# Optimization experiments

Measured on AMD Instinct MI355X. Metric: run time of the kernel, lower is better.

The kernel has to match this reference:

```python
import jax, jax.numpy as jnp
import numpy as np

EMB = 768
N_HEADS = 12
HEAD_DIM = EMB // N_HEADS


def setup_inputs() -> dict:
    key = jax.random.key(0)
    k_x, k_w1, k_b1, k_w2, k_b2 = jax.random.split(key, 5)
    B, T = 8, 1024
    s = 0.02
    return {
        "x": jax.random.normal(k_x, (B, T, EMB), dtype=jnp.float32),
        "w_attn": jax.random.normal(k_w1, (EMB, 3 * EMB), dtype=jnp.float32) * s,
        "b_attn": jax.random.normal(k_b1, (3 * EMB,), dtype=jnp.float32) * s,
        "w_proj": jax.random.normal(k_w2, (EMB, EMB), dtype=jnp.float32) * s,
        "b_proj": jax.random.normal(k_b2, (EMB,), dtype=jnp.float32) * s,
    }


def reference(x, w_attn, b_attn, w_proj, b_proj):
    B, T, C = x.shape
    qkv = x @ w_attn + b_attn                       # [B,T,3C]
    q, k, v = jnp.split(qkv, 3, axis=2)
    # [B,T,C] -> [B,H,T,D]
    q = q.reshape(B, T, N_HEADS, HEAD_DIM).transpose(0, 2, 1, 3)
    k = k.reshape(B, T, N_HEADS, HEAD_DIM).transpose(0, 2, 1, 3)
    v = v.reshape(B, T, N_HEADS, HEAD_DIM).transpose(0, 2, 1, 3)
    scale = HEAD_DIM ** -0.5
    att = jnp.einsum("bhqd,bhkd->bhqk", q, k) * scale  # [B,H,T,T]
    causal = jnp.tril(jnp.ones((T, T), dtype=bool))
    att = jnp.where(causal, att, -jnp.inf)
    att = jax.nn.softmax(att, axis=-1)
    out = jnp.einsum("bhqk,bhkd->bhqd", att, v)        # [B,H,T,D]
    out = out.transpose(0, 2, 1, 3).reshape(B, T, C)
    return out @ w_proj + b_proj
```

## Files before the change

kernel.cpp:

```cpp
#include <hip/hip_runtime.h>
#include <hip/hip_bf16.h>
#include <math.h>

#define BATCH 8
#define SEQ   1024
#define EMB   768
#define NH    12
#define HD    64
#define QKVW  (3 * EMB)
#define VOFF  (2 * EMB)

typedef short short8   __attribute__((ext_vector_type(8)));
typedef float floatx4  __attribute__((ext_vector_type(4)));

__device__ __forceinline__ short f2bf(float f) {
    union { float f; unsigned u; } v; v.f = f;
    unsigned r = (v.u + 0x7fffu + ((v.u >> 16) & 1u)) >> 16;
    return (short)r;
}

__device__ __forceinline__ void async_load16(const void* g, void* l) {
    __builtin_amdgcn_global_load_lds(
        (const __attribute__((address_space(1))) unsigned int*)g,
        (__attribute__((address_space(3))) unsigned int*)l, 16, 0, 0);
}

__global__ __launch_bounds__(256) void cvt_bf16(
    const float* __restrict__ in, short* __restrict__ out, int n8)
{
    const int i = blockIdx.x * 256 + threadIdx.x;
    if (i >= n8) return;
    const float4 a = ((const float4*)in)[2 * i];
    const float4 b = ((const float4*)in)[2 * i + 1];
    short8 s;
    s[0] = f2bf(a.x); s[1] = f2bf(a.y); s[2] = f2bf(a.z); s[3] = f2bf(a.w);
    s[4] = f2bf(b.x); s[5] = f2bf(b.y); s[6] = f2bf(b.z); s[7] = f2bf(b.w);
    ((short8*)out)[i] = s;
}

__global__ __launch_bounds__(256) void transpose_to_bf16(
    const float* __restrict__ in, short* __restrict__ outT, int R, int C)
{
    __shared__ float t[32][33];
    const int c0 = blockIdx.x * 32, r0 = blockIdx.y * 32;
    const int lx = threadIdx.x & 31, ly = threadIdx.x >> 5;
    #pragma unroll
    for (int i = 0; i < 32; i += 8)
        t[ly + i][lx] = in[(size_t)(r0 + ly + i) * C + c0 + lx];
    __syncthreads();
    #pragma unroll
    for (int i = 0; i < 32; i += 8)
        outT[(size_t)(c0 + ly + i) * R + r0 + lx] = f2bf(t[lx][ly + i]);
}

#define GBK 64

template <int MODE>
__global__ __launch_bounds__(256) void gemm_bf16(
    const short* __restrict__ A, const short* __restrict__ Bt,
    const float* __restrict__ bias, void* __restrict__ Cout,
    short* __restrict__ vt, int M, int N, int K)
{
    __shared__ __align__(16) short As[128 * GBK];
    __shared__ __align__(16) short Bs[128 * GBK];

    const int tid  = threadIdx.x;
    const int wave = tid >> 6;
    const int lane = tid & 63;
    const int ln15 = lane & 15;
    const int quad = lane >> 4;
    const int wr   = (wave >> 1) * 64;
    const int wc   = (wave & 1) * 64;
    const int row0 = blockIdx.y * 128;
    const int col0 = blockIdx.x * 128;

    const bool trans = (MODE == 0) || (col0 < VOFF);

    floatx4 acc[4][4];
    #pragma unroll
    for (int i = 0; i < 4; ++i)
        #pragma unroll
        for (int j = 0; j < 4; ++j) acc[i][j] = (floatx4){0.f, 0.f, 0.f, 0.f};

    for (int k0 = 0; k0 < K; k0 += GBK) {
        __syncthreads();
        #pragma unroll
        for (int p = 0; p < 4; ++p) {
            const int id  = p * 256 + tid;
            const int row = id >> 3;
            const int c   = (id & 7) ^ (row & 7);
            async_load16(A  + (size_t)(row0 + row) * K + k0 + c * 8, &As[id * 8]);
            async_load16(Bt + (size_t)(col0 + row) * K + k0 + c * 8, &Bs[id * 8]);
        }
        __syncthreads();

        #pragma unroll
        for (int half = 0; half < 2; ++half) {
            short8 af[4], bf[4];
            #pragma unroll
            for (int t = 0; t < 4; ++t) {
                const int ch = ((quad + half * 4) ^ (ln15 & 7)) * 8;
                af[t] = *(const short8*)&As[(wr + t * 16 + ln15) * GBK + ch];
                bf[t] = *(const short8*)&Bs[(wc + t * 16 + ln15) * GBK + ch];
            }
            if (trans) {
                #pragma unroll
                for (int i = 0; i < 4; ++i)
                    #pragma unroll
                    for (int j = 0; j < 4; ++j)
                        acc[i][j] = __builtin_amdgcn_mfma_f32_16x16x32_bf16(bf[j], af[i], acc[i][j], 0, 0, 0);
            } else {
                #pragma unroll
                for (int i = 0; i < 4; ++i)
                    #pragma unroll
                    for (int j = 0; j < 4; ++j)
                        acc[i][j] = __builtin_amdgcn_mfma_f32_16x16x32_bf16(af[i], bf[j], acc[i][j], 0, 0, 0);
            }
        }
    }

    if (MODE == 1 && !trans) {
        #pragma unroll
        for (int j = 0; j < 4; ++j) {
            const int c  = col0 + wc + j * 16 + ln15;
            const float bv = bias[c];
            const int c2 = c - VOFF;
            #pragma unroll
            for (int i = 0; i < 4; ++i) {
                const int r = row0 + wr + i * 16 + quad * 4;
                union { short s[4]; unsigned long long u; } pk;
                #pragma unroll
                for (int reg = 0; reg < 4; ++reg)
                    pk.s[reg] = f2bf(acc[i][j][reg] + bv);
                *(unsigned long long*)&vt[(size_t)(r >> 10) * (EMB * SEQ) +
                                          (size_t)c2 * SEQ + (r & 1023)] = pk.u;
            }
        }
    } else {
        float4 b4[4];
        #pragma unroll
        for (int j = 0; j < 4; ++j)
            b4[j] = *(const float4*)&bias[col0 + wc + j * 16 + quad * 4];
        #pragma unroll
        for (int i = 0; i < 4; ++i) {
            const int r = row0 + wr + i * 16 + ln15;
            #pragma unroll
            for (int j = 0; j < 4; ++j) {
                const int c = col0 + wc + j * 16 + quad * 4;
                if (MODE == 1) {
                    union { short s[4]; unsigned long long u; } pk;
                    pk.s[0] = f2bf(acc[i][j][0] + b4[j].x);
                    pk.s[1] = f2bf(acc[i][j][1] + b4[j].y);
                    pk.s[2] = f2bf(acc[i][j][2] + b4[j].z);
                    pk.s[3] = f2bf(acc[i][j][3] + b4[j].w);
                    *(unsigned long long*)&((short*)Cout)[(size_t)r * N + c] = pk.u;
                } else {
                    float4 v;
                    v.x = acc[i][j][0] + b4[j].x;
                    v.y = acc[i][j][1] + b4[j].y;
                    v.z = acc[i][j][2] + b4[j].z;
                    v.w = acc[i][j][3] + b4[j].w;
                    *(float4*)&((float*)Cout)[(size_t)r * N + c] = v;
                }
            }
        }
    }
}

#define NT12 (EMB / 64)

#define BAR()    do { asm volatile("" ::: "memory"); __builtin_amdgcn_s_barrier(); \
                      asm volatile("" ::: "memory"); } while (0)
#define LGKM0()  asm volatile("s_waitcnt lgkmcnt(0)" ::: "memory")
#define VMC0()   asm volatile("s_waitcnt vmcnt(0)" ::: "memory")
#define VMC8()   asm volatile("s_waitcnt vmcnt(8)" ::: "memory")
#define SCHED0() __builtin_amdgcn_sched_barrier(0)
#define PRIO1()  __builtin_amdgcn_s_setprio(1)
#define PRIO0()  __builtin_amdgcn_s_setprio(0)

#define LDA(bf_, r_, q_) (*(const short8*)&As[bf_][(r_) * 64 + ((((q_)) ^ ((r_) & 7)) << 3)])
#define LDB(bf_, r_, q_) (*(const short8*)&Bs[bf_][(r_) * 64 + ((((q_)) ^ ((r_) & 7)) << 3)])

#define MMA_T(IB, JB)                                                        \
    _Pragma("unroll")                                                        \
    for (int kk = 0; kk < 2; ++kk)                                           \
        _Pragma("unroll")                                                    \
        for (int mi = 0; mi < 4; ++mi)                                       \
            _Pragma("unroll")                                                \
            for (int nj = 0; nj < 2; ++nj)                                   \
                acc[(IB) + mi][(JB) + nj] =                                  \
                    __builtin_amdgcn_mfma_f32_16x16x32_bf16(                 \
                        b[(JB) + nj][kk], a[mi][kk],                         \
                        acc[(IB) + mi][(JB) + nj], 0, 0, 0);

#define MMA_D(IB, JB)                                                        \
    _Pragma("unroll")                                                        \
    for (int kk = 0; kk < 2; ++kk)                                           \
        _Pragma("unroll")                                                    \
        for (int mi = 0; mi < 4; ++mi)                                       \
            _Pragma("unroll")                                                \
            for (int nj = 0; nj < 2; ++nj)                                   \
                acc[(IB) + mi][(JB) + nj] =                                  \
                    __builtin_amdgcn_mfma_f32_16x16x32_bf16(                 \
                        a[mi][kk], b[(JB) + nj][kk],                         \
                        acc[(IB) + mi][(JB) + nj], 0, 0, 0);

#define KLOOP(MM)                                                            \
    for (int kt = 0; kt < NT12; ++kt) {                                      \
        const int buf = kt & 1;                                              \
                    \
        _Pragma("unroll")                                                    \
        for (int mi = 0; mi < 4; ++mi)                                       \
            _Pragma("unroll")                                                \
            for (int kk = 0; kk < 2; ++kk)                                   \
                a[mi][kk] = LDA(buf, ar0 + mi * 16, quad + kk * 4);          \
        _Pragma("unroll")                                                    \
        for (int nj = 0; nj < 2; ++nj)                                       \
            _Pragma("unroll")                                                \
            for (int kk = 0; kk < 2; ++kk)                                   \
                b[nj][kk] = LDB(buf, br0 + nj * 16, quad + kk * 4);          \
        BAR(); LGKM0(); SCHED0();                                            \
        PRIO1(); MM(0, 0); PRIO0();                                          \
        BAR();                                                               \
                                    \
        _Pragma("unroll")                                                    \
        for (int nj = 2; nj < 4; ++nj)                                       \
            _Pragma("unroll")                                                \
            for (int kk = 0; kk < 2; ++kk)                                   \
                b[nj][kk] = LDB(buf, br0 + nj * 16, quad + kk * 4);          \
        BAR(); LGKM0(); SCHED0();                                            \
        PRIO1(); MM(0, 2); PRIO0();                                          \
        BAR();                                                               \
             \
        _Pragma("unroll")                                                    \
        for (int mi = 0; mi < 4; ++mi)                                       \
            _Pragma("unroll")                                                \
            for (int kk = 0; kk < 2; ++kk)                                   \
                a[mi][kk] = LDA(buf, ar0 + 64 + mi * 16, quad + kk * 4);     \
        stage_half(kt + 2, 2); stage_half(kt + 2, 3);                        \
        BAR(); LGKM0(); SCHED0();                                            \
        PRIO1(); MM(4, 2); PRIO0();                                          \
        BAR();                                                               \
                           \
        stage_half(kt + 2, 0); stage_half(kt + 2, 1);                        \
        SCHED0();                                                            \
        PRIO1(); MM(4, 0); PRIO0();                                          \
        if (kt + 2 < NT12) { VMC8(); } else { VMC0(); }                      \
        BAR();                                                               \
    }

__global__ __launch_bounds__(512, 2) void gemm_qkv_256(
    const short* __restrict__ A, const short* __restrict__ Bt,
    const float* __restrict__ bias, short* __restrict__ qkvb,
    short* __restrict__ vt)
{
    __shared__ __align__(16) short As[2][256 * 64];
    __shared__ __align__(16) short Bs[2][256 * 64];

    const int tid  = threadIdx.x;
    const int wave = tid >> 6;
    const int lane = tid & 63;
    const int ln15 = lane & 15;
    const int quad = lane >> 4;
    const int wm   = wave >> 2;
    const int wn   = wave & 3;

    const int orig = blockIdx.x;
    const int wg   = (orig & 7) * 36 + (orig >> 3);
    const int bx   = wg % (QKVW / 256);
    const int by   = wg / (QKVW / 256);
    const int row0 = by * 256;
    const int col0 = bx * 256;
    const bool vpath = (col0 >= VOFF);

    const short* Ag = A  + (size_t)row0 * EMB;
    const short* Bg = Bt + (size_t)col0 * EMB;

    auto stage_half = [&](int t, int h) {
        if (t >= NT12) return;
        const int buf   = t & 1;
        const int k0    = t * 64;
        const int rbase = (h & 1) * 128;
        short* lb       = (h < 2) ? &As[buf][rbase * 64] : &Bs[buf][rbase * 64];
        const short* gb = (h < 2) ? Ag : Bg;
        #pragma unroll
        for (int p = 0; p < 2; ++p) {
            const int id  = p * 512 + tid;
            const int row = rbase + (id >> 3);
            const int c   = (id & 7) ^ (row & 7);
            async_load16(gb + (size_t)row * EMB + k0 + c * 8, lb + (size_t)id * 8);
        }
    };

    floatx4 acc[8][4];
    #pragma unroll
    for (int i = 0; i < 8; ++i)
        #pragma unroll
        for (int j = 0; j < 4; ++j) acc[i][j] = (floatx4){0.f, 0.f, 0.f, 0.f};

    short8 a[4][2];
    short8 b[4][2];

    #pragma unroll
    for (int h = 0; h < 4; ++h) stage_half(0, h);
    #pragma unroll
    for (int h = 0; h < 4; ++h) stage_half(1, h);
    VMC8();
    BAR();

    const int ar0 = wm * 128 + ln15;
    const int br0 = wn * 64 + ln15;

    if (vpath) { KLOOP(MMA_D) } else { KLOOP(MMA_T) }

    if (!vpath) {
        #pragma unroll
        for (int j = 0; j < 4; ++j) {
            const float4 b4 = *(const float4*)&bias[col0 + wn * 64 + j * 16 + quad * 4];
            #pragma unroll
            for (int i = 0; i < 8; ++i) {
                const int r = row0 + wm * 128 + i * 16 + ln15;
                const int c = col0 + wn * 64 + j * 16 + quad * 4;
                union { short s[4]; unsigned long long u; } pk;
                pk.s[0] = f2bf(acc[i][j][0] + b4.x);
                pk.s[1] = f2bf(acc[i][j][1] + b4.y);
                pk.s[2] = f2bf(acc[i][j][2] + b4.z);
                pk.s[3] = f2bf(acc[i][j][3] + b4.w);
                *(unsigned long long*)&qkvb[(size_t)r * QKVW + c] = pk.u;
            }
        }
    } else {
        #pragma unroll
        for (int j = 0; j < 4; ++j) {
            const int c  = col0 + wn * 64 + j * 16 + ln15;
            const float bv = bias[c];
            const int c2 = c - VOFF;
            #pragma unroll
            for (int i = 0; i < 8; ++i) {
                const int r = row0 + wm * 128 + i * 16 + quad * 4;
                union { short s[4]; unsigned long long u; } pk;
                #pragma unroll
                for (int reg = 0; reg < 4; ++reg)
                    pk.s[reg] = f2bf(acc[i][j][reg] + bv);
                *(unsigned long long*)&vt[(size_t)(r >> 10) * (EMB * SEQ) +
                                          (size_t)c2 * SEQ + (r & 1023)] = pk.u;
            }
        }
    }
}

#define LDK 72

__global__ __launch_bounds__(256) void attn_mfma(
    const short* __restrict__ qkv, const short* __restrict__ vt,
    short* __restrict__ out)
{
    __shared__ __align__(16) short Ks[64 * LDK];
    __shared__ __align__(16) short Vt[64 * LDK];
    __shared__ __align__(16) short Ps[4 * 16 * LDK];

    const int tid  = threadIdx.x;
    const int wave = tid >> 6;
    const int lane = tid & 63;
    const int ln15 = lane & 15;
    const int quad = lane >> 4;

    const int qc = 15 - (int)(blockIdx.x / (BATCH * NH));
    const int bh = blockIdx.x % (BATCH * NH);
    const int h  = bh % NH;
    const int b  = bh / NH;

    const int q0w = qc * 64 + wave * 16;

    const short* qkv_b = qkv + (size_t)b * SEQ * QKVW + h * HD;
    const short* Kg  = qkv_b + EMB;
    const short* Vtg = vt + ((size_t)b * EMB + h * HD) * SEQ;

    short8 qf[2];
    {
        const short* qrow = qkv_b + (size_t)(q0w + ln15) * QKVW;
        qf[0] = *(const short8*)(qrow + quad * 8);
        qf[1] = *(const short8*)(qrow + quad * 8 + 32);
    }

    floatx4 o[4];
    #pragma unroll
    for (int i = 0; i < 4; ++i) o[i] = (floatx4){0.f, 0.f, 0.f, 0.f};
    float lp[4] = {0.f, 0.f, 0.f, 0.f};

    const int rr = tid >> 3;
    const int c8 = (tid & 7) * 8;

    for (int kt = 0; kt <= qc; ++kt) {
        #pragma unroll
        for (int p = 0; p < 2; ++p) {
            const int r2 = rr + p * 32;
            *(uint4*)&Ks[r2 * LDK + c8] =
                *(const uint4*)(Kg + (size_t)(kt * 64 + r2) * QKVW + c8);
            *(uint4*)&Vt[r2 * LDK + c8] =
                *(const uint4*)(Vtg + (size_t)r2 * SEQ + kt * 64 + c8);
        }
        __syncthreads();

        floatx4 s[4];
        #pragma unroll
        for (int i = 0; i < 4; ++i) s[i] = (floatx4){0.f, 0.f, 0.f, 0.f};
        #pragma unroll
        for (int st = 0; st < 2; ++st)
            #pragma unroll
            for (int sub = 0; sub < 4; ++sub) {
                const short8 kf = *(const short8*)&Ks[(ln15 + sub * 16) * LDK + quad * 8 + st * 32];
                s[sub] = __builtin_amdgcn_mfma_f32_16x16x32_bf16(qf[st], kf, s[sub], 0, 0, 0);
            }

        const bool diag = (kt == qc);
        #pragma unroll
        for (int sub = 0; sub < 4; ++sub)
            #pragma unroll
            for (int reg = 0; reg < 4; ++reg) {
                float pv = __expf(s[sub][reg] * 0.125f);
                if (diag && (ln15 + sub * 16 > wave * 16 + quad * 4 + reg)) pv = 0.f;
                s[sub][reg] = pv;
            }
        #pragma unroll
        for (int reg = 0; reg < 4; ++reg)
            lp[reg] += (s[0][reg] + s[1][reg]) + (s[2][reg] + s[3][reg]);

        short* Pw = &Ps[wave * 16 * LDK];
        #pragma unroll
        for (int sub = 0; sub < 4; ++sub)
            #pragma unroll
            for (int reg = 0; reg < 4; ++reg) {
                const int qr   = quad * 4 + reg;
                const int kr8  = sub * 2 + (ln15 >> 3);
                const int slot = (kr8 + 5 * quad + reg) & 7;
                Pw[qr * LDK + slot * 8 + (ln15 & 7)] = f2bf(s[sub][reg]);
            }

        short8 pf[2];
        #pragma unroll
        for (int st = 0; st < 2; ++st) {
            const int slot = ((quad + 4 * st) + 5 * (ln15 >> 2) + (ln15 & 3)) & 7;
            pf[st] = *(const short8*)&Pw[ln15 * LDK + slot * 8];
        }

        #pragma unroll
        for (int st = 0; st < 2; ++st)
            #pragma unroll
            for (int sub = 0; sub < 4; ++sub) {
                const short8 vf = *(const short8*)&Vt[(ln15 + sub * 16) * LDK + quad * 8 + st * 32];
                o[sub] = __builtin_amdgcn_mfma_f32_16x16x32_bf16(pf[st], vf, o[sub], 0, 0, 0);
            }

        __syncthreads();
    }

    #pragma unroll
    for (int reg = 0; reg < 4; ++reg) {
        float t = lp[reg];
        #pragma unroll
        for (int off = 1; off <= 8; off <<= 1)
            t += __shfl_xor(t, off, 64);
        const float inv = 1.0f / t;
        const size_t row = (size_t)(b * SEQ + q0w + quad * 4 + reg) * EMB + h * HD;
        #pragma unroll
        for (int sub = 0; sub < 4; ++sub)
            out[row + ln15 + sub * 16] = f2bf(o[sub][reg] * inv);
    }
}

extern "C" void kernel_launch(void* const* d_in, const int* in_sizes, int n_in,
                              void* d_out, int out_size, void* d_ws, size_t ws_size,
                              hipStream_t stream)
{
    const float* x      = (const float*)d_in[0];
    const float* w_attn = (const float*)d_in[1];
    const float* b_attn = (const float*)d_in[2];
    const float* w_proj = (const float*)d_in[3];
    const float* b_proj = (const float*)d_in[4];
    float* out = (float*)d_out;

    const int M = BATCH * SEQ;

    short* xb    = (short*)d_ws;
    short* waT   = xb    + (size_t)M * EMB;
    short* wpT   = waT   + (size_t)QKVW * EMB;
    short* qkvb  = wpT   + (size_t)EMB * EMB;
    short* vtb   = qkvb  + (size_t)M * QKVW;
    short* attnb = vtb   + (size_t)BATCH * EMB * SEQ;

    dim3 blk(256);

    cvt_bf16<<<dim3((M * EMB) / 8 / 256), blk, 0, stream>>>(x, xb, (M * EMB) / 8);
    transpose_to_bf16<<<dim3(QKVW / 32, EMB / 32), blk, 0, stream>>>(w_attn, waT, EMB, QKVW);
    transpose_to_bf16<<<dim3(EMB / 32, EMB / 32), blk, 0, stream>>>(w_proj, wpT, EMB, EMB);

    gemm_qkv_256<<<dim3((QKVW / 256) * (M / 256)), dim3(512), 0, stream>>>(
        xb, waT, b_attn, qkvb, vtb);

    attn_mfma<<<dim3(16 * BATCH * NH), blk, 0, stream>>>(qkvb, vtb, attnb);

    gemm_bf16<0><<<dim3(EMB / 128, M / 128), blk, 0, stream>>>(
        attnb, wpT, b_proj, out, nullptr, M, EMB, EMB);
}
```

Before: 216.1 us.

## Replace projection GEMM with double-buffered 128x192 tile kernel using six waves

The output projection GEMM moves from a simple single-buffered 128x128 kernel with 4 waves to a new kernel with 128x192 tiles, 6 waves, and double-buffered LDS. Loads for the next K tile are staged asynchronously and overlap the MFMA work through split A/B staging, explicit waitcnt and barriers, and priority hints. Workgroup IDs are also remapped for L2 locality. The goal is to hide global-load latency and improve data reuse. The cost is more LDS per block and fragile hand-written synchronisation.

```diff
diff --git a/kernel.cpp b/kernel.cpp
--- a/kernel.cpp
+++ b/kernel.cpp
@@ -53,130 +53,18 @@
         outT[(size_t)(c0 + ly + i) * R + r0 + lx] = f2bf(t[lx][ly + i]);
 }
 
-#define GBK 64
-
-template <int MODE>
-__global__ __launch_bounds__(256) void gemm_bf16(
-    const short* __restrict__ A, const short* __restrict__ Bt,
-    const float* __restrict__ bias, void* __restrict__ Cout,
-    short* __restrict__ vt, int M, int N, int K)
-{
-    __shared__ __align__(16) short As[128 * GBK];
-    __shared__ __align__(16) short Bs[128 * GBK];
-
-    const int tid  = threadIdx.x;
-    const int wave = tid >> 6;
-    const int lane = tid & 63;
-    const int ln15 = lane & 15;
-    const int quad = lane >> 4;
-    const int wr   = (wave >> 1) * 64;
-    const int wc   = (wave & 1) * 64;
-    const int row0 = blockIdx.y * 128;
-    const int col0 = blockIdx.x * 128;
-
-    const bool trans = (MODE == 0) || (col0 < VOFF);
-
-    floatx4 acc[4][4];
-    #pragma unroll
-    for (int i = 0; i < 4; ++i)
-        #pragma unroll
-        for (int j = 0; j < 4; ++j) acc[i][j] = (floatx4){0.f, 0.f, 0.f, 0.f};
-
-    for (int k0 = 0; k0 < K; k0 += GBK) {
-        __syncthreads();
-        #pragma unroll
-        for (int p = 0; p < 4; ++p) {
-            const int id  = p * 256 + tid;
-            const int row = id >> 3;
-            const int c   = (id & 7) ^ (row & 7);
-            async_load16(A  + (size_t)(row0 + row) * K + k0 + c * 8, &As[id * 8]);
-            async_load16(Bt + (size_t)(col0 + row) * K + k0 + c * 8, &Bs[id * 8]);
-        }
-        __syncthreads();
-
-        #pragma unroll
-        for (int half = 0; half < 2; ++half) {
-            short8 af[4], bf[4];
-            #pragma unroll
-            for (int t = 0; t < 4; ++t) {
-                const int ch = ((quad + half * 4) ^ (ln15 & 7)) * 8;
-                af[t] = *(const short8*)&As[(wr + t * 16 + ln15) * GBK + ch];
-                bf[t] = *(const short8*)&Bs[(wc + t * 16 + ln15) * GBK + ch];
-            }
-            if (trans) {
-                #pragma unroll
-                for (int i = 0; i < 4; ++i)
-                    #pragma unroll
-                    for (int j = 0; j < 4; ++j)
-                        acc[i][j] = __builtin_amdgcn_mfma_f32_16x16x32_bf16(bf[j], af[i], acc[i][j], 0, 0, 0);
-            } else {
-                #pragma unroll
-                for (int i = 0; i < 4; ++i)
-                    #pragma unroll
-                    for (int j = 0; j < 4; ++j)
-                        acc[i][j] = __builtin_amdgcn_mfma_f32_16x16x32_bf16(af[i], bf[j], acc[i][j], 0, 0, 0);
-            }
-        }
-    }
-
-    if (MODE == 1 && !trans) {
-        #pragma unroll
-        for (int j = 0; j < 4; ++j) {
-            const int c  = col0 + wc + j * 16 + ln15;
-            const float bv = bias[c];
-            const int c2 = c - VOFF;
-            #pragma unroll
-            for (int i = 0; i < 4; ++i) {
-                const int r = row0 + wr + i * 16 + quad * 4;
-                union { short s[4]; unsigned long long u; } pk;
-                #pragma unroll
-                for (int reg = 0; reg < 4; ++reg)
-                    pk.s[reg] = f2bf(acc[i][j][reg] + bv);
-                *(unsigned long long*)&vt[(size_t)(r >> 10) * (EMB * SEQ) +
-                                          (size_t)c2 * SEQ + (r & 1023)] = pk.u;
-            }
-        }
-    } else {
-        float4 b4[4];
-        #pragma unroll
-        for (int j = 0; j < 4; ++j)
-            b4[j] = *(const float4*)&bias[col0 + wc + j * 16 + quad * 4];
-        #pragma unroll
-        for (int i = 0; i < 4; ++i) {
-            const int r = row0 + wr + i * 16 + ln15;
-            #pragma unroll
-            for (int j = 0; j < 4; ++j) {
-                const int c = col0 + wc + j * 16 + quad * 4;
-                if (MODE == 1) {
-                    union { short s[4]; unsigned long long u; } pk;
-                    pk.s[0] = f2bf(acc[i][j][0] + b4[j].x);
-                    pk.s[1] = f2bf(acc[i][j][1] + b4[j].y);
-                    pk.s[2] = f2bf(acc[i][j][2] + b4[j].z);
-                    pk.s[3] = f2bf(acc[i][j][3] + b4[j].w);
-                    *(unsigned long long*)&((short*)Cout)[(size_t)r * N + c] = pk.u;
-                } else {
-                    float4 v;
-                    v.x = acc[i][j][0] + b4[j].x;
-                    v.y = acc[i][j][1] + b4[j].y;
-                    v.z = acc[i][j][2] + b4[j].z;
-                    v.w = acc[i][j][3] + b4[j].w;
-                    *(float4*)&((float*)Cout)[(size_t)r * N + c] = v;
-                }
-            }
-        }
-    }
-}
-
 #define NT12 (EMB / 64)
 
 #define BAR()    do { asm volatile("" ::: "memory"); __builtin_amdgcn_s_barrier(); \
                       asm volatile("" ::: "memory"); } while (0)
 #define LGKM0()  asm volatile("s_waitcnt lgkmcnt(0)" ::: "memory")
 #define VMC0()   asm volatile("s_waitcnt vmcnt(0)" ::: "memory")
+#define VMC4()   asm volatile("s_waitcnt vmcnt(4)" ::: "memory")
 #define VMC8()   asm volatile("s_waitcnt vmcnt(8)" ::: "memory")
 #define SCHED0() __builtin_amdgcn_sched_barrier(0)
 #define PRIO1()  __builtin_amdgcn_s_setprio(1)
 #define PRIO0()  __builtin_amdgcn_s_setprio(0)
+
 
 #define LDA(bf_, r_, q_) (*(const short8*)&As[bf_][(r_) * 64 + ((((q_)) ^ ((r_) & 7)) << 3)])
 #define LDB(bf_, r_, q_) (*(const short8*)&Bs[bf_][(r_) * 64 + ((((q_)) ^ ((r_) & 7)) << 3)])
@@ -349,6 +237,143 @@
     }
 }
 
+
+#define LDA8(bf_, r_, q_) (*(const short8*)&As[bf_][(r_) * 64 + ((((q_)) ^ ((r_) & 7)) << 3)])
+#define LDB8(bf_, r_, q_) (*(const short8*)&Bs[bf_][(r_) * 64 + ((((q_)) ^ ((r_) & 7)) << 3)])
+
+#define MMA_T2(JB)                                                           \
+    _Pragma("unroll")                                                        \
+    for (int kk = 0; kk < 2; ++kk)                                           \
+        _Pragma("unroll")                                                    \
+        for (int mi = 0; mi < 4; ++mi)                                       \
+            _Pragma("unroll")                                                \
+            for (int nj = 0; nj < 2; ++nj)                                   \
+                acc[mi][(JB) + nj] =                                         \
+                    __builtin_amdgcn_mfma_f32_16x16x32_bf16(                 \
+                        b[(JB) + nj][kk], a[mi][kk],                         \
+                        acc[mi][(JB) + nj], 0, 0, 0);
+
+#define KLOOP2(MM)                                                           \
+    for (int kt = 0; kt < NT12; ++kt) {                                      \
+        const int buf = kt & 1;                                              \
+                 \
+        _Pragma("unroll")                                                    \
+        for (int mi = 0; mi < 4; ++mi)                                       \
+            _Pragma("unroll")                                                \
+            for (int kk = 0; kk < 2; ++kk)                                   \
+                a[mi][kk] = LDA8(buf, ar0 + mi * 16, quad + kk * 4);         \
+        _Pragma("unroll")                                                    \
+        for (int nj = 0; nj < 2; ++nj)                                       \
+            _Pragma("unroll")                                                \
+            for (int kk = 0; kk < 2; ++kk)                                   \
+                b[nj][kk] = LDB8(buf, br0 + nj * 16, quad + kk * 4);         \
+        if (kt + 1 < NT12) stage_B(kt + 1);                                  \
+        BAR(); LGKM0(); SCHED0();                                            \
+        PRIO1(); MM(0); PRIO0();                                             \
+        BAR();                                                               \
+                     \
+        _Pragma("unroll")                                                    \
+        for (int nj = 2; nj < 4; ++nj)                                       \
+            _Pragma("unroll")                                                \
+            for (int kk = 0; kk < 2; ++kk)                                   \
+                b[nj][kk] = LDB8(buf, br0 + nj * 16, quad + kk * 4);         \
+        if (kt + 2 < NT12) stage_A(kt + 2);                                  \
+        BAR(); LGKM0(); SCHED0();                                            \
+        PRIO1(); MM(2); PRIO0();                                             \
+        if (kt + 2 < NT12) {                                                 \
+            if (wuni < 4) { VMC4(); } else { VMC0(); }                       \
+        } else if (kt + 1 < NT12) { VMC0(); }                                \
+        BAR();                                                               \
+    }
+
+__global__ __launch_bounds__(384, 3) void gemm_proj(
+    const short* __restrict__ A, const short* __restrict__ Bt,
+    const float* __restrict__ bias, float* __restrict__ Cout,
+    int N, int nbx)
+{
+    __shared__ __align__(16) short As[2][128 * 64];
+    __shared__ __align__(16) short Bs[2][192 * 64];
+
+    const int tid  = threadIdx.x;
+    const int wave = tid >> 6;
+    const int lane = tid & 63;
+    const int ln15 = lane & 15;
+    const int quad = lane >> 4;
+    const int wm   = wave / 3;
+    const int wn   = wave % 3;
+    const int wuni = __builtin_amdgcn_readfirstlane(wave);
+
+    const int orig = blockIdx.x;
+    const int wg   = (orig & 7) * (8 * nbx) + (orig >> 3);
+    const int bx   = wg % nbx;
+    const int by   = wg / nbx;
+    const int row0 = by * 128;
+    const int col0 = bx * 192;
+
+    const short* Ag = A  + (size_t)row0 * EMB;
+    const short* Bg = Bt + (size_t)col0 * EMB;
+
+    auto stage_A = [&](int t) {
+        if (wave >= 4) return;
+        const int buf = t & 1;
+        #pragma unroll
+        for (int p = 0; p < 4; ++p) {
+            const int id  = (wave * 4 + p) * 64 + lane;
+            const int row = id >> 3;
+            const int c   = (id & 7) ^ (row & 7);
+            async_load16(Ag + (size_t)row * EMB + t * 64 + c * 8, &As[buf][id * 8]);
+        }
+    };
+    auto stage_B = [&](int t) {
+        const int buf = t & 1;
+        #pragma unroll
+        for (int p = 0; p < 4; ++p) {
+            const int id  = (wave * 4 + p) * 64 + lane;
+            const int row = id >> 3;
+            const int c   = (id & 7) ^ (row & 7);
+            async_load16(Bg + (size_t)row * EMB + t * 64 + c * 8, &Bs[buf][id * 8]);
+        }
+    };
+
+    floatx4 acc[4][4];
+    #pragma unroll
+    for (int i = 0; i < 4; ++i)
+        #pragma unroll
+        for (int j = 0; j < 4; ++j) acc[i][j] = (floatx4){0.f, 0.f, 0.f, 0.f};
+
+    short8 a[4][2];
+    short8 b[4][2];
+
+    stage_A(0); stage_B(0); stage_A(1);
+    if (wuni < 4) { VMC4(); } else { VMC0(); }
+    BAR();
+
+    const int ar0 = wm * 64 + ln15;
+    const int br0 = wn * 64 + ln15;
+
+    KLOOP2(MMA_T2)
+
+    const int wr = wm * 64, wc = wn * 64;
+    float4 b4[4];
+    #pragma unroll
+    for (int j = 0; j < 4; ++j)
+        b4[j] = *(const float4*)&bias[col0 + wc + j * 16 + quad * 4];
+    #pragma unroll
+    for (int i = 0; i < 4; ++i) {
+        const int r = row0 + wr + i * 16 + ln15;
+        #pragma unroll
+        for (int j = 0; j < 4; ++j) {
+            const int c = col0 + wc + j * 16 + quad * 4;
+            float4 v;
+            v.x = acc[i][j][0] + b4[j].x;
+            v.y = acc[i][j][1] + b4[j].y;
+            v.z = acc[i][j][2] + b4[j].z;
+            v.w = acc[i][j][3] + b4[j].w;
+            *(float4*)&Cout[(size_t)r * N + c] = v;
+        }
+    }
+}
+
 #define LDK 72
 
 __global__ __launch_bounds__(256) void attn_mfma(
@@ -500,6 +525,6 @@
 
     attn_mfma<<<dim3(16 * BATCH * NH), blk, 0, stream>>>(qkvb, vtb, attnb);
 
-    gemm_bf16<0><<<dim3(EMB / 128, M / 128), blk, 0, stream>>>(
-        attnb, wpT, b_proj, out, nullptr, M, EMB, EMB);
-}
+    gemm_proj<<<dim3((M / 128) * (EMB / 192)), dim3(384), 0, stream>>>(
+        attnb, wpT, b_proj, out, EMB, EMB / 192);
+}
```

New measurement: 212.7 us. No clear change (-1.6%).
